# Kernel optimization log

Measured on AMD Instinct MI355X. Metric: run time of the kernel, lower is better.

Reference implementation:

```python
import jax, jax.numpy as jnp
import numpy as np


def setup_inputs() -> dict:
    key = jax.random.key(0)
    k1, k2, k3 = jax.random.split(key, 3)
    B, D, T = 16, 64, 8192
    n_codebook, n_emb = 4, 512
    z_e_x = jax.random.normal(k1, (B, D, T), dtype=jnp.float32)
    # torch init is uniform(-1/n_emb, 1/n_emb)
    codebook = jax.random.uniform(k2, (n_codebook, D, n_emb), dtype=jnp.float32,
                                  minval=-1.0 / n_emb, maxval=1.0 / n_emb)
    codebook_index = jax.random.randint(k3, (1,), 0, n_codebook, dtype=jnp.int64)
    return {"z_e_x": z_e_x, "codebook": codebook, "codebook_index": codebook_index}


def reference(z_e_x, codebook, codebook_index):
    # codebook: [n_codebook, D, n_emb]; select one codebook -> [D, n_emb]
    cb = codebook[codebook_index[0]]
    B, D, T = z_e_x.shape
    # [B, D, T] -> [B*T, D]
    z = jnp.transpose(z_e_x, (0, 2, 1)).reshape(-1, D)
    # squared L2 distances to each code: [B*T, n_emb]
    dist2 = (jnp.sum(z * z, axis=1, keepdims=True)
             - 2.0 * (z @ cb)
             + jnp.sum(cb * cb, axis=0))
    z_id_flat = jnp.argmax(-dist2, axis=1)          # nearest code index, [B*T]
    z_id = z_id_flat.reshape(B, T)
    z_q = cb.T[z_id_flat].reshape(B, T, D)          # gather codes
    z_q = jnp.transpose(z_q, (0, 2, 1))             # [B, D, T]
    return z_q, z_id
```

## Files before the change

### kernel.cpp

```cpp
#include <hip/hip_runtime.h>


constexpr int Dc = 64, Ec = 512, Tc = 8192;
constexpr int QTOT = 131072, ZQ = 8388608;
constexpr int QPB = 256;
constexpr int NBLK = QTOT / QPB;

using half8  = __attribute__((ext_vector_type(8))) _Float16;
using f32x16 = __attribute__((ext_vector_type(16))) float;

__global__ void vq_prep(const float* __restrict__ cbfull, const int* __restrict__ cbidx,
                        _Float16* __restrict__ wsf) {
    int tid = blockIdx.x * 256 + threadIdx.x;
    const float* cb = cbfull + (size_t)(cbidx[0] & 3) * (Dc * Ec);
    if (tid < 512) {
        float c = cb[tid];
        float a = __fmul_rn(c, c);
        for (int d = 1; d < Dc; ++d) { c = cb[d * Ec + tid]; a = __fadd_rn(a, __fmul_rn(c, c)); }
        ((float*)(wsf + 32768))[tid] = a;
    }
    if (tid >= 4096) return;
    int l = tid & 63, c = (tid >> 6) & 3, g = tid >> 8;
    int n = g * 32 + (l & 31);
    int kbase = c * 16 + (l >> 5) * 8;
    _Float16* dst = wsf + (size_t)(g * 4 + c) * 512 + l * 8;
    #pragma unroll
    for (int i = 0; i < 8; ++i)
        dst[i] = (_Float16)(cb[(kbase + i) * Ec + n] * 512.0f);
}

__global__ __launch_bounds__(512) void vq_main(
    const float* __restrict__ z, const float* __restrict__ cbfull,
    const int* __restrict__ cbidx, const _Float16* __restrict__ wsf,
    float* __restrict__ out) {
    __shared__ __attribute__((aligned(16))) _Float16 s_frag[32768];
    __shared__ float s_c2[Ec];
    __shared__ unsigned s_w[QPB];
    __shared__ int s_idx[QPB];

    const int tid = threadIdx.x;
    const int lane = tid & 63;
    const int wave = __builtin_amdgcn_readfirstlane(tid >> 6);
    const int col = lane & 31, hh = lane >> 5;
    const int q0 = blockIdx.x * QPB;
    const int b = q0 >> 13, t0 = q0 & (Tc - 1);
    const int myq = wave * 32 + col;
    const int t = t0 + myq;

    const int ci = cbidx[0] & 3;
    const float* __restrict__ cb = cbfull + (size_t)ci * (Dc * Ec);

    {
        const uint4* src = (const uint4*)wsf;
        uint4* dst = (uint4*)s_frag;
        #pragma unroll
        for (int k = 0; k < 8; ++k) dst[tid + k * 512] = src[tid + k * 512];
    }
    if (tid < 512) s_c2[tid] = ((const float*)(wsf + 32768))[tid];

    float zv[32];
    const float* zp = z + (size_t)b * Dc * Tc + t;
    #pragma unroll
    for (int c = 0; c < 4; ++c)
        #pragma unroll
        for (int i = 0; i < 8; ++i)
            zv[c * 8 + i] = zp[(size_t)(c * 16 + hh * 8 + i) * Tc];

    float s1p = 0.f;
    #pragma unroll
    for (int e = 0; e < 32; ++e) s1p = __fmaf_rn(zv[e], zv[e], s1p);
    float s1b = (s1p + __shfl_xor(s1p, 32, 64)) * 1.001f + 0.01f;
    float wf = 2.5e-7f * (s1b + 1.f) + 3.2e-5f * sqrtf(s1b) + 1e-5f;
    unsigned w_int = (s1b > 880.f) ? 0x7FFFFFFFu : (unsigned)(wf * 2.147483648e9f) + 512u;
    if (hh == 0) s_w[myq] = w_int;

    half8 uhf[4], ulf[4];
    #pragma unroll
    for (int c = 0; c < 4; ++c)
        #pragma unroll
        for (int i = 0; i < 8; ++i) {
            float f = -16.0f * zv[c * 8 + i];
            _Float16 h = (_Float16)f;
            float hf = (float)h;
            uhf[c][i] = h;
            ulf[c][i] = (_Float16)(f - hf);
        }

    __syncthreads();

    unsigned m1[16], m2[16];
    #pragma unroll
    for (int r = 0; r < 16; ++r) { m1[r] = 0xFFFFFFFFu; m2[r] = 0xFFFFFFFFu; }

    #pragma unroll 2
    for (int g = 0; g < 16; ++g) {
        const float kb = s_c2[g * 32 + col] * 4096.0f;
        f32x16 acc;
        #pragma unroll
        for (int r = 0; r < 16; ++r) acc[r] = kb;
        #pragma unroll
        for (int c = 0; c < 4; ++c) {
            half8 chf = *(const half8*)(s_frag + (size_t)(g * 4 + c) * 512 + lane * 8);
            acc = __builtin_amdgcn_mfma_f32_32x32x16_f16(uhf[c], chf, acc, 0, 0, 0);
            acc = __builtin_amdgcn_mfma_f32_32x32x16_f16(ulf[c], chf, acc, 0, 0, 0);
        }
        const unsigned jj = (unsigned)(g * 32 + col);
        #pragma unroll
        for (int r = 0; r < 16; ++r) {
            float keyf = __fmaf_rn(acc[r], 2.44140625e-4f, 3.0f);
            unsigned key = (__float_as_uint(keyf) << 9) | jj;
            unsigned mx = key > m1[r] ? key : m1[r];
            m1[r] = key < m1[r] ? key : m1[r];
            m2[r] = mx < m2[r] ? mx : m2[r];
        }
    }

    #pragma unroll
    for (int st = 1; st < 32; st <<= 1) {
        #pragma unroll
        for (int r = 0; r < 16; ++r) {
            unsigned o1 = __shfl_xor(m1[r], st, 64);
            unsigned o2 = __shfl_xor(m2[r], st, 64);
            unsigned mx = m1[r] > o1 ? m1[r] : o1;
            m1[r] = m1[r] < o1 ? m1[r] : o1;
            m2[r] = m2[r] < o2 ? m2[r] : o2;
            m2[r] = m2[r] < mx ? m2[r] : mx;
        }
    }

    unsigned F1 = 0xFFFFFFFFu, F2 = 0xFFFFFFFFu;
    #pragma unroll
    for (int r = 0; r < 16; ++r) if (col == r) { F1 = m1[r]; F2 = m2[r]; }
    bool amb = false;
    if (col < 16) {
        int row = (col & 3) + 8 * (col >> 2) + 4 * hh;
        int Q = wave * 32 + row;
        s_idx[Q] = (int)(F1 & 511u);
        unsigned wq = s_w[Q];
        amb = ((unsigned long long)F2 <= (unsigned long long)F1 + wq);
    }
    unsigned long long mask = __ballot(amb);

    while (mask) {
        int L = __ffsll(mask) - 1; mask &= mask - 1;
        int r = L & 31, hb = L >> 5;
        int Q = wave * 32 + (r & 3) + 8 * (r >> 2) + 4 * hb;
        const float* zq = z + (size_t)b * Dc * Tc + (t0 + Q);
        float zr[64];
        #pragma unroll
        for (int d = 0; d < 64; ++d) zr[d] = zq[(size_t)d * Tc];
        float rr[8];
        #pragma unroll
        for (int u = 0; u < 8; ++u) rr[u] = __fmul_rn(zr[u], zr[u]);
        #pragma unroll
        for (int i = 8; i < 64; i += 8)
            #pragma unroll
            for (int u = 0; u < 8; ++u)
                rr[u] = __fadd_rn(rr[u], __fmul_rn(zr[i + u], zr[i + u]));
        float s1 = __fadd_rn(__fadd_rn(__fadd_rn(rr[0], rr[1]), __fadd_rn(rr[2], rr[3])),
                             __fadd_rn(__fadd_rn(rr[4], rr[5]), __fadd_rn(rr[6], rr[7])));
        float bk = __int_as_float(0x7f800000);
        int bj = 0;
        for (int u = 0; u < 8; ++u) {
            int j = u * 64 + lane;
            float G = 0.f;
            #pragma unroll
            for (int d = 0; d < 64; ++d) G = __fmaf_rn(zr[d], cb[d * Ec + j], G);
            float key = __fadd_rn(__fsub_rn(s1, __fmul_rn(2.0f, G)), s_c2[j]);
            if (key < bk) { bk = key; bj = j; }
        }
        #pragma unroll
        for (int m = 1; m < 64; m <<= 1) {
            float pk = __shfl_xor(bk, m, 64);
            int pj = __shfl_xor(bj, m, 64);
            if (pk < bk || (pk == bk && pj < bj)) { bk = pk; bj = pj; }
        }
        if (lane == 0) s_idx[Q] = bj;
    }
    __syncthreads();

    #pragma unroll
    for (int qh = 0; qh < 4; ++qh) {
        const int ql = qh * 64 + lane;
        const int jj = s_idx[ql];
        const int tt = t0 + ql;
        float* op = out + ((size_t)b * Dc + wave * 8) * Tc + tt;
        #pragma unroll
        for (int dd = 0; dd < 8; ++dd)
            op[(size_t)dd * Tc] = cb[(wave * 8 + dd) * Ec + jj];
        if (wave == 0) out[ZQ + q0 + ql] = (float)jj;
    }
}

extern "C" void kernel_launch(void* const* d_in, const int* in_sizes, int n_in,
                              void* d_out, int out_size, void* d_ws, size_t ws_size,
                              hipStream_t stream) {
    const float* z = (const float*)d_in[0];
    const float* cbfull = (const float*)d_in[1];
    const int* cbidx = (const int*)d_in[2];
    _Float16* wsf = (_Float16*)d_ws;
    float* out = (float*)d_out;

    hipLaunchKernelGGL(vq_prep, dim3(16), dim3(256), 0, stream, cbfull, cbidx, wsf);
    hipLaunchKernelGGL(vq_main, dim3(NBLK), dim3(512), 0, stream,
                       z, cbfull, cbidx, wsf, out);
}
```

Baseline: 105.3 us.

## Move ambiguous-query exact rescan into separate kernel and fold key bias

Instead of having the owning wave serially recompute exact FP32 distances for ambiguous queries inside the main kernel, the main kernel writes the candidate index straight out and records a per-wave ambiguity ballot in the workspace. A new lightweight rescan kernel, one 64-thread block per wave-group, then recomputes the ambiguous queries and overwrites their outputs. This is meant to remove tail latency from waves stalled on the rare slow path. It also hoists the z loads above the shared-memory fill and folds the key offset into the accumulator init, removing one FMA per element. The cost is an extra launch plus many mostly-empty blocks.

After: 113.6 us. 7.9% more time.

```diff
diff --git a/kernel.cpp b/kernel.cpp
--- a/kernel.cpp
+++ b/kernel.cpp
@@ -31,7 +31,7 @@
 
 __global__ __launch_bounds__(512) void vq_main(
     const float* __restrict__ z, const float* __restrict__ cbfull,
-    const int* __restrict__ cbidx, const _Float16* __restrict__ wsf,
+    const int* __restrict__ cbidx, _Float16* __restrict__ wsf,
     float* __restrict__ out) {
     __shared__ __attribute__((aligned(16))) _Float16 s_frag[32768];
     __shared__ float s_c2[Ec];
@@ -50,6 +50,14 @@
     const int ci = cbidx[0] & 3;
     const float* __restrict__ cb = cbfull + (size_t)ci * (Dc * Ec);
 
+    float zv[32];
+    const float* zp = z + (size_t)b * Dc * Tc + t;
+    #pragma unroll
+    for (int c = 0; c < 4; ++c)
+        #pragma unroll
+        for (int i = 0; i < 8; ++i)
+            zv[c * 8 + i] = zp[(size_t)(c * 16 + hh * 8 + i) * Tc];
+
     {
         const uint4* src = (const uint4*)wsf;
         uint4* dst = (uint4*)s_frag;
@@ -57,14 +65,6 @@
         for (int k = 0; k < 8; ++k) dst[tid + k * 512] = src[tid + k * 512];
     }
     if (tid < 512) s_c2[tid] = ((const float*)(wsf + 32768))[tid];
-
-    float zv[32];
-    const float* zp = z + (size_t)b * Dc * Tc + t;
-    #pragma unroll
-    for (int c = 0; c < 4; ++c)
-        #pragma unroll
-        for (int i = 0; i < 8; ++i)
-            zv[c * 8 + i] = zp[(size_t)(c * 16 + hh * 8 + i) * Tc];
 
     float s1p = 0.f;
     #pragma unroll
@@ -94,7 +94,7 @@
 
     #pragma unroll 2
     for (int g = 0; g < 16; ++g) {
-        const float kb = s_c2[g * 32 + col] * 4096.0f;
+        const float kb = __fmaf_rn(s_c2[g * 32 + col], 4096.0f, 12288.0f);
         f32x16 acc;
         #pragma unroll
         for (int r = 0; r < 16; ++r) acc[r] = kb;
@@ -107,8 +107,7 @@
         const unsigned jj = (unsigned)(g * 32 + col);
         #pragma unroll
         for (int r = 0; r < 16; ++r) {
-            float keyf = __fmaf_rn(acc[r], 2.44140625e-4f, 3.0f);
-            unsigned key = (__float_as_uint(keyf) << 9) | jj;
+            unsigned key = (__float_as_uint(acc[r]) << 9) | jj;
             unsigned mx = key > m1[r] ? key : m1[r];
             m1[r] = key < m1[r] ? key : m1[r];
             m2[r] = mx < m2[r] ? mx : m2[r];
@@ -139,13 +138,44 @@
         unsigned wq = s_w[Q];
         amb = ((unsigned long long)F2 <= (unsigned long long)F1 + wq);
     }
-    unsigned long long mask = __ballot(amb);
+    unsigned long long bal = __ballot(amb);
+    if (lane == 0)
+        ((unsigned long long*)(wsf + 33792))[blockIdx.x * 8 + wave] = bal;
+    __syncthreads();
+
+    #pragma unroll
+    for (int qh = 0; qh < 4; ++qh) {
+        const int ql = qh * 64 + lane;
+        const int jj = s_idx[ql];
+        const int tt = t0 + ql;
+        float* op = out + ((size_t)b * Dc + wave * 8) * Tc + tt;
+        #pragma unroll
+        for (int dd = 0; dd < 8; ++dd)
+            op[(size_t)dd * Tc] = cb[(wave * 8 + dd) * Ec + jj];
+        if (wave == 0) out[ZQ + q0 + ql] = (float)jj;
+    }
+}
+
+__global__ __launch_bounds__(64) void vq_rescan(
+    const float* __restrict__ z, const float* __restrict__ cbfull,
+    const int* __restrict__ cbidx, const _Float16* __restrict__ wsf,
+    float* __restrict__ out) {
+    const int lane = threadIdx.x;
+    unsigned long long mask = ((const unsigned long long*)(wsf + 33792))[blockIdx.x];
+    if (mask == 0) return;
+
+    const int ci = cbidx[0] & 3;
+    const float* __restrict__ cb = cbfull + (size_t)ci * (Dc * Ec);
+    const float* __restrict__ c2g = (const float*)(wsf + 32768);
+    const int qbase = (blockIdx.x >> 3) * QPB + (blockIdx.x & 7) * 32;
+    const int b = qbase >> 13, tb = qbase & (Tc - 1);
 
     while (mask) {
         int L = __ffsll(mask) - 1; mask &= mask - 1;
         int r = L & 31, hb = L >> 5;
-        int Q = wave * 32 + (r & 3) + 8 * (r >> 2) + 4 * hb;
-        const float* zq = z + (size_t)b * Dc * Tc + (t0 + Q);
+        int row = (r & 3) + 8 * (r >> 2) + 4 * hb;
+        int q = qbase + row, t = tb + row;
+        const float* zq = z + (size_t)b * Dc * Tc + t;
         float zr[64];
         #pragma unroll
         for (int d = 0; d < 64; ++d) zr[d] = zq[(size_t)d * Tc];
@@ -166,7 +196,7 @@
             float G = 0.f;
             #pragma unroll
             for (int d = 0; d < 64; ++d) G = __fmaf_rn(zr[d], cb[d * Ec + j], G);
-            float key = __fadd_rn(__fsub_rn(s1, __fmul_rn(2.0f, G)), s_c2[j]);
+            float key = __fadd_rn(__fsub_rn(s1, __fmul_rn(2.0f, G)), c2g[j]);
             if (key < bk) { bk = key; bj = j; }
         }
         #pragma unroll
@@ -175,20 +205,8 @@
             int pj = __shfl_xor(bj, m, 64);
             if (pk < bk || (pk == bk && pj < bj)) { bk = pk; bj = pj; }
         }
-        if (lane == 0) s_idx[Q] = bj;
-    }
-    __syncthreads();
-
-    #pragma unroll
-    for (int qh = 0; qh < 4; ++qh) {
-        const int ql = qh * 64 + lane;
-        const int jj = s_idx[ql];
-        const int tt = t0 + ql;
-        float* op = out + ((size_t)b * Dc + wave * 8) * Tc + tt;
-        #pragma unroll
-        for (int dd = 0; dd < 8; ++dd)
-            op[(size_t)dd * Tc] = cb[(wave * 8 + dd) * Ec + jj];
-        if (wave == 0) out[ZQ + q0 + ql] = (float)jj;
+        out[((size_t)b * Dc + lane) * Tc + t] = cb[lane * Ec + bj];
+        if (lane == 0) out[ZQ + q] = (float)bj;
     }
 }
 
@@ -202,6 +220,6 @@
     float* out = (float*)d_out;
 
     hipLaunchKernelGGL(vq_prep, dim3(16), dim3(256), 0, stream, cbfull, cbidx, wsf);
-    hipLaunchKernelGGL(vq_main, dim3(NBLK), dim3(512), 0, stream,
-                       z, cbfull, cbidx, wsf, out);
-}
+    hipLaunchKernelGGL(vq_main, dim3(NBLK), dim3(512), 0, stream, z, cbfull, cbidx, wsf, out);
+    hipLaunchKernelGGL(vq_rescan, dim3(NBLK * 8), dim3(64), 0, stream, z, cbfull, cbidx, wsf, out);
+}
```
